# Performance work log

Measured on AMD Instinct MI355X. Metric: run time of the kernel, lower is better.

The kernel has to match this reference:

```python
import jax, jax.numpy as jnp
import numpy as np
from jax import lax

EPS = 1e-6
CLAMP = 1e4


def _ln_last(x, w, b):
    # fp32 LayerNorm over last dim
    mu = jnp.mean(x, axis=-1, keepdims=True)
    var = jnp.mean(jnp.square(x - mu), axis=-1, keepdims=True)
    return (x - mu) * lax.rsqrt(var + EPS) * w + b


def _nan_clean(x):
    return jnp.nan_to_num(x, nan=0.0, posinf=CLAMP, neginf=-CLAMP)


def setup_inputs() -> dict:
    key = jax.random.key(0)
    B, C, H, W = 4, 256, 64, 64
    hid = 2 * C  # expand=2
    k = 3        # d_conv
    ks = jax.random.split(key, 12)
    s = 0.02
    return {
        "x": jax.random.normal(ks[0], (B, C, H, W), jnp.float32),
        "ln2d_w": jnp.ones((C,), jnp.float32),
        "ln2d_b": jnp.zeros((C,), jnp.float32),
        "inproj_w": jax.random.normal(ks[1], (C, C), jnp.float32) * s,
        "inproj_b": jnp.zeros((C,), jnp.float32),
        "dw2d_w": jax.random.normal(ks[2], (C, 3, 3), jnp.float32) * s,
        "dw2d_b": jnp.zeros((C,), jnp.float32),
        "ssm_ln_w": jnp.ones((C,), jnp.float32),
        "ssm_ln_b": jnp.zeros((C,), jnp.float32),
        "ssm_in_w": jax.random.normal(ks[3], (2 * hid, C), jnp.float32) * s,
        "ssm_in_b": jnp.zeros((2 * hid,), jnp.float32),
        "ssm_dw_w": jax.random.normal(ks[4], (hid, k), jnp.float32) * s,
        "ssm_dw_b": jnp.zeros((hid,), jnp.float32),
        "ssm_out_w": jax.random.normal(ks[5], (C, hid), jnp.float32) * s,
        "ssm_out_b": jnp.zeros((C,), jnp.float32),
        "outproj_w": jax.random.normal(ks[6], (C, C), jnp.float32) * s,
        "outproj_b": jnp.zeros((C,), jnp.float32),
    }


def reference(x, ln2d_w, ln2d_b, inproj_w, inproj_b, dw2d_w, dw2d_b,
              ssm_ln_w, ssm_ln_b, ssm_in_w, ssm_in_b, ssm_dw_w, ssm_dw_b,
              ssm_out_w, ssm_out_b, outproj_w, outproj_b):
    B, C, H, W = x.shape
    L = H * W

    # LN2d over channel dim (per-pixel LN on C)
    y = _ln_last(x.transpose(0, 2, 3, 1), ln2d_w, ln2d_b).transpose(0, 3, 1, 2)

    # 1x1 conv in_proj
    y = jnp.einsum('bchw,oc->bohw', y, inproj_w) + inproj_b[None, :, None, None]

    # depthwise 3x3 conv, SAME padding
    y = lax.conv_general_dilated(
        y, dw2d_w[:, None, :, :], (1, 1), ((1, 1), (1, 1)),
        dimension_numbers=('NCHW', 'OIHW', 'NCHW'),
        feature_group_count=C) + dw2d_b[None, :, None, None]

    # cross-scan: 4 routes (B,L,C)
    s0 = y.reshape(B, C, L).transpose(0, 2, 1)                      # row-major
    s1 = s0[:, ::-1]                                                # reversed
    s2 = y.transpose(0, 1, 3, 2).reshape(B, C, L).transpose(0, 2, 1)  # col-major
    s3 = s2[:, ::-1]
    s = jnp.concatenate([s0, s1, s2, s3], axis=0)  # (4B, L, C), shared SSM weights

    # MambaOrLite fallback: LN -> GLU -> depthwise conv1d -> out proj + residual
    r = _ln_last(s, ssm_ln_w, ssm_ln_b)
    r = r @ ssm_in_w.T + ssm_in_b                   # (4B, L, 2*hid)
    a, g = jnp.split(r, 2, axis=-1)
    r = a * jax.nn.sigmoid(g)                       # (4B, L, hid)
    r = r.transpose(0, 2, 1)                        # (4B, hid, L)
    hid = r.shape[1]
    k = ssm_dw_w.shape[-1]
    pad = ((k - 1) // 2, k // 2)
    r = lax.conv_general_dilated(
        r, ssm_dw_w[:, None, :], (1,), (pad,),
        dimension_numbers=('NCH', 'OIH', 'NCH'),
        feature_group_count=hid) + ssm_dw_b[None, :, None]
    r = r.transpose(0, 2, 1) @ ssm_out_w.T + ssm_out_b  # (4B, L, C)
    ys = _nan_clean(r) + s

    # cross-merge: average the 4 routes back to (B,C,H,W)
    y0, y1, y2, y3 = jnp.split(ys, 4, axis=0)
    m0 = y0.transpose(0, 2, 1).reshape(B, C, H, W)
    m1 = y1[:, ::-1].transpose(0, 2, 1).reshape(B, C, H, W)
    m2 = y2.transpose(0, 2, 1).reshape(B, C, W, H).transpose(0, 1, 3, 2)
    m3 = y3[:, ::-1].transpose(0, 2, 1).reshape(B, C, W, H).transpose(0, 1, 3, 2)
    m = (m0 + m1 + m2 + m3) * 0.25

    out = jnp.einsum('bchw,oc->bohw', m, outproj_w) + outproj_b[None, :, None, None]
    out = _nan_clean(out)
    return out + x
```

## Files before the change

### kernel.cpp

```cpp
#include <hip/hip_runtime.h>

typedef float f32x4 __attribute__((ext_vector_type(4)));
typedef __bf16 bf16x8 __attribute__((ext_vector_type(8)));
typedef unsigned short u16;
typedef unsigned int u32;

__device__ __forceinline__ float bf2f(u32 b) {
  u32 x = (b & 0xffffu) << 16;
  return __builtin_bit_cast(float, x);
}
__device__ __forceinline__ u16 f2bf(float f) {
  u32 x = __builtin_bit_cast(u32, f);
  x += 0x7fffu + ((x >> 16) & 1u);
  return (u16)(x >> 16);
}
__device__ __forceinline__ void gload16(const void* g, void* l) {
  __builtin_amdgcn_global_load_lds((__attribute__((address_space(1))) void*)g,
                                   (__attribute__((address_space(3))) void*)l,
                                   16, 0, 0);
}

__global__ __launch_bounds__(256, 2)
void k_ln2d_prep(const float* __restrict__ x, const float* __restrict__ lw,
                 const float* __restrict__ lb, u16* __restrict__ A,
                 const float* __restrict__ inproj_w, const float* __restrict__ ssm_in_w,
                 const float* __restrict__ ssm_out_w, const float* __restrict__ outproj_w,
                 const float* __restrict__ dw2d_w, const float* __restrict__ ssm_dw_w,
                 const float* __restrict__ ssm_dw_b, const float* __restrict__ ssm_out_b,
                 u16* __restrict__ w1b, u16* __restrict__ w2b, u16* __restrict__ w3b,
                 u16* __restrict__ w4b, float* __restrict__ cvec, float* __restrict__ wT9,
                 float* __restrict__ w02, float* __restrict__ w14) {
  __shared__ float T[256 * 65];
  __shared__ float ps1[4][64], ps2[4][64];
  __shared__ float mu[64], rsd[64];
  int bid = blockIdx.x, tid = threadIdx.x;
  if (bid >= 256) {
    int pb = bid - 256;
    if (pb < 512) {
      const float* s; u16* d; int base;
      if (pb < 256)      { s = ssm_in_w;  d = w2b; base = pb; }
      else if (pb < 384) { s = ssm_out_w; d = w3b; base = pb - 256; }
      else if (pb < 448) { s = inproj_w;  d = w1b; base = pb - 384; }
      else               { s = outproj_w; d = w4b; base = pb - 448; }
      int i = base * 1024 + tid * 4;
      float4 v = *(const float4*)&s[i];
      u32 a = (u32)f2bf(v.x) | ((u32)f2bf(v.y) << 16);
      u32 b = (u32)f2bf(v.z) | ((u32)f2bf(v.w) << 16);
      *(uint2*)&d[i] = make_uint2(a, b);
    } else if (pb == 512) {
      float s = ssm_out_b[tid];
      const float* wr = ssm_out_w + (size_t)tid * 512;
      #pragma unroll 8
      for (int k = 0; k < 512; ++k) s += ssm_dw_b[k] * wr[k];
      cvec[tid] = s;
    } else {
      #pragma unroll
      for (int j = 0; j < 9; ++j) wT9[j * 256 + tid] = dw2d_w[tid * 9 + j];
      #pragma unroll
      for (int q = 0; q < 2; ++q) {
        int c = tid + q * 256;
        w02[c] = ssm_dw_w[c * 3 + 0] + ssm_dw_w[c * 3 + 2];
        w14[c] = 4.f * ssm_dw_w[c * 3 + 1];
      }
    }
    return;
  }
  int wv = tid >> 6, lane = tid & 63;
  int cq = lane >> 4, p4 = (lane & 15) * 4;
  int n0 = bid * 64, bb = n0 >> 12, hw0 = n0 & 4095;
  const float* xb = x + ((size_t)bb << 20);
  float s0 = 0, s1 = 0, s2 = 0, s3 = 0;
  float q0 = 0, q1 = 0, q2 = 0, q3 = 0;
  #pragma unroll 4
  for (int i = 0; i < 16; ++i) {
    int c = wv * 64 + i * 4 + cq;
    float4 v = *(const float4*)&xb[((size_t)c << 12) + hw0 + p4];
    T[c * 65 + p4 + 0] = v.x; T[c * 65 + p4 + 1] = v.y;
    T[c * 65 + p4 + 2] = v.z; T[c * 65 + p4 + 3] = v.w;
    s0 += v.x; s1 += v.y; s2 += v.z; s3 += v.w;
    q0 += v.x * v.x; q1 += v.y * v.y; q2 += v.z * v.z; q3 += v.w * v.w;
  }
  #pragma unroll
  for (int off = 16; off < 64; off <<= 1) {
    s0 += __shfl_xor(s0, off); s1 += __shfl_xor(s1, off);
    s2 += __shfl_xor(s2, off); s3 += __shfl_xor(s3, off);
    q0 += __shfl_xor(q0, off); q1 += __shfl_xor(q1, off);
    q2 += __shfl_xor(q2, off); q3 += __shfl_xor(q3, off);
  }
  if (cq == 0) {
    ps1[wv][p4 + 0] = s0; ps1[wv][p4 + 1] = s1; ps1[wv][p4 + 2] = s2; ps1[wv][p4 + 3] = s3;
    ps2[wv][p4 + 0] = q0; ps2[wv][p4 + 1] = q1; ps2[wv][p4 + 2] = q2; ps2[wv][p4 + 3] = q3;
  }
  __syncthreads();
  if (tid < 64) {
    float S1 = ps1[0][tid] + ps1[1][tid] + ps1[2][tid] + ps1[3][tid];
    float S2 = ps2[0][tid] + ps2[1][tid] + ps2[2][tid] + ps2[3][tid];
    float m = S1 * (1.f / 256.f);
    float var = S2 * (1.f / 256.f) - m * m;
    mu[tid] = m;
    rsd[tid] = rsqrtf(var + 1e-6f);
  }
  __syncthreads();
  int c4b = (tid & 15) * 4, p2b = tid >> 4;
  #pragma unroll
  for (int cc = 0; cc < 4; ++cc) {
    int c4 = cc * 64 + c4b;
    float4 w4 = *(const float4*)&lw[c4];
    float4 g4 = *(const float4*)&lb[c4];
    #pragma unroll
    for (int i2 = 0; i2 < 4; ++i2) {
      int p2 = p2b + 16 * i2;
      float m = mu[p2], rs = rsd[p2];
      float o0 = (T[(c4 + 0) * 65 + p2] - m) * rs * w4.x + g4.x;
      float o1 = (T[(c4 + 1) * 65 + p2] - m) * rs * w4.y + g4.y;
      float o2 = (T[(c4 + 2) * 65 + p2] - m) * rs * w4.z + g4.z;
      float o3 = (T[(c4 + 3) * 65 + p2] - m) * rs * w4.w + g4.w;
      u32 a = (u32)f2bf(o0) | ((u32)f2bf(o1) << 16);
      u32 b = (u32)f2bf(o2) | ((u32)f2bf(o3) << 16);
      *(uint2*)&A[(size_t)(n0 + p2) * 256 + c4] = make_uint2(a, b);
    }
  }
}

__global__ __launch_bounds__(256)
void k_dw3x3_ln(const u16* __restrict__ Y1, const float* __restrict__ wT,
                const float* __restrict__ dwb, const float* __restrict__ lnw,
                const float* __restrict__ lnb, u16* __restrict__ Yc,
                u16* __restrict__ A) {
  int tid = threadIdx.x;
  int n = blockIdx.x * 4 + (tid >> 6);
  int lane = tid & 63;
  int c0 = lane * 4;
  int b = n >> 12, hw = n & 4095, h = hw >> 6, w = hw & 63;
  float4 b4 = *(const float4*)&dwb[c0];
  float a0 = b4.x, a1 = b4.y, a2 = b4.z, a3 = b4.w;
  #pragma unroll
  for (int ky = 0; ky < 3; ++ky) {
    int hh = h + ky - 1;
    if (hh < 0 || hh > 63) continue;
    #pragma unroll
    for (int kx = 0; kx < 3; ++kx) {
      int ww = w + kx - 1;
      if (ww < 0 || ww > 63) continue;
      size_t nn = ((size_t)b << 12) + (hh << 6) + ww;
      uint2 u = *(const uint2*)&Y1[nn * 256 + c0];
      float4 w4 = *(const float4*)&wT[(ky * 3 + kx) * 256 + c0];
      a0 += bf2f(u.x) * w4.x;
      a1 += bf2f(u.x >> 16) * w4.y;
      a2 += bf2f(u.y) * w4.z;
      a3 += bf2f(u.y >> 16) * w4.w;
    }
  }
  u32 p0 = (u32)f2bf(a0) | ((u32)f2bf(a1) << 16);
  u32 p1 = (u32)f2bf(a2) | ((u32)f2bf(a3) << 16);
  *(uint2*)&Yc[(size_t)n * 256 + c0] = make_uint2(p0, p1);
  float s1 = a0 + a1 + a2 + a3;
  float s2 = a0 * a0 + a1 * a1 + a2 * a2 + a3 * a3;
  #pragma unroll
  for (int off = 1; off < 64; off <<= 1) {
    s1 += __shfl_xor(s1, off);
    s2 += __shfl_xor(s2, off);
  }
  float m = s1 * (1.f / 256.f);
  float var = s2 * (1.f / 256.f) - m * m;
  float rs = rsqrtf(var + 1e-6f);
  float4 w4 = *(const float4*)&lnw[c0];
  float4 g4 = *(const float4*)&lnb[c0];
  float o0 = (a0 - m) * rs * w4.x + g4.x;
  float o1 = (a1 - m) * rs * w4.y + g4.y;
  float o2 = (a2 - m) * rs * w4.z + g4.z;
  float o3 = (a3 - m) * rs * w4.w + g4.w;
  u32 qa = (u32)f2bf(o0) | ((u32)f2bf(o1) << 16);
  u32 qb = (u32)f2bf(o2) | ((u32)f2bf(o3) << 16);
  *(uint2*)&A[(size_t)n * 256 + c0] = make_uint2(qa, qb);
}

template <int EPI>
__global__ __launch_bounds__(256, 4)
void k_gemm2(const u16* __restrict__ R, const u16* __restrict__ Cm,
             const float* __restrict__ bias, int K, int nCt, int ldo,
             u16* __restrict__ outb, float* __restrict__ outf,
             const float* __restrict__ resf) {
  __shared__ u16 tR[2][64 * 32];
  __shared__ u16 tC[2][128 * 32];
  int tid = threadIdx.x, lane = tid & 63, wv = tid >> 6;
  int rt = blockIdx.x / nCt, ct = blockIdx.x % nCt;
  int r0 = rt * 64, c0 = ct * 128;
  int fr = lane & 15, kc = lane >> 4;
  int sr = lane >> 2, sc = (lane & 3) * 8;
  f32x4 acc[4][2] = {};
  int nK = K >> 5;
  const u16* gR  = R  + (size_t)(r0 + wv * 16 + sr) * K + sc;
  const u16* gC0 = Cm + (size_t)(c0 + wv * 32 + sr) * K + sc;
  const u16* gC1 = Cm + (size_t)(c0 + wv * 32 + 16 + sr) * K + sc;
  auto STAGE = [&](int buf, int kt) {
    int k0 = kt * 32;
    gload16(gR + k0,  &tR[buf][wv * 16 * 32]);
    gload16(gC0 + k0, &tC[buf][(wv * 32) * 32]);
    gload16(gC1 + k0, &tC[buf][(wv * 32 + 16) * 32]);
  };
  auto COMPUTE = [&](int buf) {
    bf16x8 af[4], wf[2];
    #pragma unroll
    for (int m = 0; m < 4; ++m)
      af[m] = *(const bf16x8*)&tR[buf][(m * 16 + fr) * 32 + kc * 8];
    #pragma unroll
    for (int n = 0; n < 2; ++n)
      wf[n] = *(const bf16x8*)&tC[buf][(wv * 32 + n * 16 + fr) * 32 + kc * 8];
    #pragma unroll
    for (int m = 0; m < 4; ++m)
      #pragma unroll
      for (int n = 0; n < 2; ++n)
        acc[m][n] = __builtin_amdgcn_mfma_f32_16x16x32_bf16(af[m], wf[n], acc[m][n], 0, 0, 0);
  };
  STAGE(0, 0);
  __syncthreads();
  int cur = 0;
  for (int kt = 0; kt < nK - 1; ++kt) {
    STAGE(cur ^ 1, kt + 1);
    __builtin_amdgcn_sched_barrier(0);
    COMPUTE(cur);
    __syncthreads();
    cur ^= 1;
  }
  COMPUTE(cur);
  #pragma unroll
  for (int m = 0; m < 4; ++m) {
    #pragma unroll
    for (int n = 0; n < 2; ++n) {
      #pragma unroll
      for (int r = 0; r < 4; ++r) {
        float v = acc[m][n][r];
        if (EPI == 0) {
          int gn = r0 + m * 16 + kc * 4 + r;
          int go = c0 + wv * 32 + n * 16 + fr;
          outb[(size_t)gn * ldo + go] = f2bf(v + bias[go]);
        } else {
          int go = r0 + m * 16 + kc * 4 + r;
          int gn = c0 + wv * 32 + n * 16 + fr;
          int b = gn >> 12, hw = gn & 4095;
          size_t idx = (((size_t)(b * 256 + go)) << 12) + hw;
          outf[idx] = v + bias[go] + resf[idx];
        }
      }
    }
  }
}

__global__ __launch_bounds__(256, 3)
void k_gate2(const u16* __restrict__ A, const u16* __restrict__ W,
             const float* __restrict__ bias, u16* __restrict__ G) {
  __shared__ u16 tR[2][64 * 32];
  __shared__ u16 tCa[2][128 * 32];
  __shared__ u16 tCg[2][128 * 32];
  int tid = threadIdx.x, lane = tid & 63, wv = tid >> 6;
  int rt = blockIdx.x >> 2, ot = blockIdx.x & 3;
  int r0 = rt * 64, o0 = ot * 128;
  int fr = lane & 15, kc = lane >> 4;
  int sr = lane >> 2, sc = (lane & 3) * 8;
  const int K = 256;
  f32x4 acca[4][2] = {}, accg[4][2] = {};
  const u16* gR  = A + (size_t)(r0 + wv * 16 + sr) * K + sc;
  const u16* gA0 = W + (size_t)(o0 + wv * 32 + sr) * K + sc;
  const u16* gA1 = W + (size_t)(o0 + wv * 32 + 16 + sr) * K + sc;
  const u16* gG0 = W + (size_t)(512 + o0 + wv * 32 + sr) * K + sc;
  const u16* gG1 = W + (size_t)(512 + o0 + wv * 32 + 16 + sr) * K + sc;
  auto STAGE = [&](int buf, int kt) {
    int k0 = kt * 32;
    gload16(gR + k0,  &tR[buf][wv * 16 * 32]);
    gload16(gA0 + k0, &tCa[buf][(wv * 32) * 32]);
    gload16(gA1 + k0, &tCa[buf][(wv * 32 + 16) * 32]);
    gload16(gG0 + k0, &tCg[buf][(wv * 32) * 32]);
    gload16(gG1 + k0, &tCg[buf][(wv * 32 + 16) * 32]);
  };
  auto COMPUTE = [&](int buf) {
    bf16x8 af[4], wa[2], wg[2];
    #pragma unroll
    for (int m = 0; m < 4; ++m)
      af[m] = *(const bf16x8*)&tR[buf][(m * 16 + fr) * 32 + kc * 8];
    #pragma unroll
    for (int n = 0; n < 2; ++n) {
      wa[n] = *(const bf16x8*)&tCa[buf][(wv * 32 + n * 16 + fr) * 32 + kc * 8];
      wg[n] = *(const bf16x8*)&tCg[buf][(wv * 32 + n * 16 + fr) * 32 + kc * 8];
    }
    #pragma unroll
    for (int m = 0; m < 4; ++m)
      #pragma unroll
      for (int n = 0; n < 2; ++n) {
        acca[m][n] = __builtin_amdgcn_mfma_f32_16x16x32_bf16(af[m], wa[n], acca[m][n], 0, 0, 0);
        accg[m][n] = __builtin_amdgcn_mfma_f32_16x16x32_bf16(af[m], wg[n], accg[m][n], 0, 0, 0);
      }
  };
  STAGE(0, 0);
  __syncthreads();
  int cur = 0;
  for (int kt = 0; kt < 7; ++kt) {
    STAGE(cur ^ 1, kt + 1);
    __builtin_amdgcn_sched_barrier(0);
    COMPUTE(cur);
    __syncthreads();
    cur ^= 1;
  }
  COMPUTE(cur);
  #pragma unroll
  for (int m = 0; m < 4; ++m) {
    #pragma unroll
    for (int n = 0; n < 2; ++n) {
      #pragma unroll
      for (int r = 0; r < 4; ++r) {
        int gn = r0 + m * 16 + kc * 4 + r;
        int go = o0 + wv * 32 + n * 16 + fr;
        float a = acca[m][n][r] + bias[go];
        float g = accg[m][n][r] + bias[512 + go];
        G[(size_t)gn * 512 + go] = f2bf(a / (1.f + expf(-g)));
      }
    }
  }
}

__global__ __launch_bounds__(256, 2)
void k_gemm_scan(const u16* __restrict__ G, const u16* __restrict__ W3,
                 const float* __restrict__ w02, const float* __restrict__ w14,
                 const float* __restrict__ cvec, const u16* __restrict__ Yc,
                 u16* __restrict__ M) {
  __shared__ u16 tR[2][32 * 32];
  __shared__ u16 tC[2][256 * 32];
  int tid = threadIdx.x, lane = tid & 63, wv = tid >> 6;
  int r0 = blockIdx.x * 32;
  int fr = lane & 15, kc = lane >> 4;
  int zrow = tid >> 3;
  int zg = (tid & 7) * 4;
  int n = r0 + zrow;
  int b = n >> 12, hw = n & 4095, h = hw >> 6, w = hw & 63;
  int m = w * 64 + h;
  int mm1 = m - 1, mp1 = m + 1;
  size_t o_c = (size_t)n * 512 + zg;
  size_t o_p = (size_t)(hw > 0 ? n - 1 : n) * 512 + zg;
  size_t o_n = (size_t)(hw < 4095 ? n + 1 : n) * 512 + zg;
  size_t o_u = (size_t)(m > 0 ? ((b << 12) + ((mm1 & 63) << 6) + (mm1 >> 6)) : n) * 512 + zg;
  size_t o_d = (size_t)(m < 4095 ? ((b << 12) + ((mp1 & 63) << 6) + (mp1 >> 6)) : n) * 512 + zg;
  float mP = hw > 0 ? 1.f : 0.f, mN = hw < 4095 ? 1.f : 0.f;
  float mU = m > 0 ? 1.f : 0.f, mD = m < 4095 ? 1.f : 0.f;
  f32x4 acc[2][4] = {};
  auto STAGE_C = [&](int buf, int kt) {
    int k0 = kt * 32;
    #pragma unroll
    for (int i = 0; i < 4; ++i) {
      int s0 = wv * 256 + i * 64;
      int s = s0 + lane;
      int row = s >> 2, off = (s & 3) * 8;
      gload16(W3 + (size_t)row * 512 + k0 + off, &tC[buf][s0 * 8]);
    }
  };
  uint2 lc, lp, ln_, lu, ld;
  float4 va, vb;
  auto ZLOAD = [&](int kt) {
    int c = kt * 32 + zg;
    lc = *(const uint2*)&G[o_c + (kt * 32)];
    lp = *(const uint2*)&G[o_p + (kt * 32)];
    ln_ = *(const uint2*)&G[o_n + (kt * 32)];
    lu = *(const uint2*)&G[o_u + (kt * 32)];
    ld = *(const uint2*)&G[o_d + (kt * 32)];
    va = *(const float4*)&w02[c];
    vb = *(const float4*)&w14[c];
  };
  auto ZSTORE = [&](int buf) {
    float s_0 = mP * bf2f(lp.x) + mN * bf2f(ln_.x) + mU * bf2f(lu.x) + mD * bf2f(ld.x);
    float s_1 = mP * bf2f(lp.x >> 16) + mN * bf2f(ln_.x >> 16) + mU * bf2f(lu.x >> 16) + mD * bf2f(ld.x >> 16);
    float s_2 = mP * bf2f(lp.y) + mN * bf2f(ln_.y) + mU * bf2f(lu.y) + mD * bf2f(ld.y);
    float s_3 = mP * bf2f(lp.y >> 16) + mN * bf2f(ln_.y >> 16) + mU * bf2f(lu.y >> 16) + mD * bf2f(ld.y >> 16);
    float z0 = va.x * s_0 + vb.x * bf2f(lc.x);
    float z1 = va.y * s_1 + vb.y * bf2f(lc.x >> 16);
    float z2 = va.z * s_2 + vb.z * bf2f(lc.y);
    float z3 = va.w * s_3 + vb.w * bf2f(lc.y >> 16);
    u32 p0 = (u32)f2bf(z0) | ((u32)f2bf(z1) << 16);
    u32 p1 = (u32)f2bf(z2) | ((u32)f2bf(z3) << 16);
    *(uint2*)&tR[buf][zrow * 32 + zg] = make_uint2(p0, p1);
  };
  auto COMPUTE = [&](int buf) {
    bf16x8 af[2], wf[4];
    #pragma unroll
    for (int mi = 0; mi < 2; ++mi)
      af[mi] = *(const bf16x8*)&tR[buf][(mi * 16 + fr) * 32 + kc * 8];
    #pragma unroll
    for (int ni = 0; ni < 4; ++ni)
      wf[ni] = *(const bf16x8*)&tC[buf][(wv * 64 + ni * 16 + fr) * 32 + kc * 8];
    #pragma unroll
    for (int mi = 0; mi < 2; ++mi)
      #pragma unroll
      for (int ni = 0; ni < 4; ++ni)
        acc[mi][ni] = __builtin_amdgcn_mfma_f32_16x16x32_bf16(af[mi], wf[ni], acc[mi][ni], 0, 0, 0);
  };
  STAGE_C(0, 0);
  ZLOAD(0);
  ZSTORE(0);
  __syncthreads();
  int cur = 0;
  for (int kt = 0; kt < 15; ++kt) {
    ZLOAD(kt + 1);
    STAGE_C(cur ^ 1, kt + 1);
    COMPUTE(cur);
    ZSTORE(cur ^ 1);
    __syncthreads();
    cur ^= 1;
  }
  COMPUTE(cur);
  #pragma unroll
  for (int mi = 0; mi < 2; ++mi) {
    #pragma unroll
    for (int ni = 0; ni < 4; ++ni) {
      #pragma unroll
      for (int r = 0; r < 4; ++r) {
        int gn = r0 + mi * 16 + kc * 4 + r;
        int go = wv * 64 + ni * 16 + fr;
        size_t idx = (size_t)gn * 256 + go;
        M[idx] = f2bf(0.25f * acc[mi][ni][r] + cvec[go] + bf2f(Yc[idx]));
      }
    }
  }
}

extern "C" void kernel_launch(void* const* d_in, const int* in_sizes, int n_in,
                              void* d_out, int out_size, void* d_ws, size_t ws_size,
                              hipStream_t stream) {
  const float* x         = (const float*)d_in[0];
  const float* ln2d_w    = (const float*)d_in[1];
  const float* ln2d_b    = (const float*)d_in[2];
  const float* inproj_w  = (const float*)d_in[3];
  const float* inproj_b  = (const float*)d_in[4];
  const float* dw2d_w    = (const float*)d_in[5];
  const float* dw2d_b    = (const float*)d_in[6];
  const float* ssm_ln_w  = (const float*)d_in[7];
  const float* ssm_ln_b  = (const float*)d_in[8];
  const float* ssm_in_w  = (const float*)d_in[9];
  const float* ssm_in_b  = (const float*)d_in[10];
  const float* ssm_dw_w  = (const float*)d_in[11];
  const float* ssm_dw_b  = (const float*)d_in[12];
  const float* ssm_out_w = (const float*)d_in[13];
  const float* ssm_out_b = (const float*)d_in[14];
  const float* outproj_w = (const float*)d_in[15];
  const float* outproj_b = (const float*)d_in[16];
  float* out = (float*)d_out;

  char* ws = (char*)d_ws;
  size_t off = 0;
  auto take = [&](size_t bytes) -> char* {
    char* p = ws + off;
    off = (off + bytes + 255) & ~(size_t)255;
    return p;
  };
  u16* w1b    = (u16*)take(65536 * 2);
  u16* w2b    = (u16*)take(262144 * 2);
  u16* w3b    = (u16*)take(131072 * 2);
  u16* w4b    = (u16*)take(65536 * 2);
  float* cvec = (float*)take(256 * 4);
  float* wT9  = (float*)take(9 * 256 * 4);
  float* w02  = (float*)take(512 * 4);
  float* w14  = (float*)take(512 * 4);
  u16* Abuf   = (u16*)take((size_t)16384 * 256 * 2);
  u16* Y1     = (u16*)take((size_t)16384 * 256 * 2);
  u16* Yc     = (u16*)take((size_t)16384 * 256 * 2);
  u16* G      = (u16*)take((size_t)16384 * 512 * 2);
  (void)ws_size; (void)in_sizes; (void)n_in; (void)out_size;

  k_ln2d_prep<<<770, 256, 0, stream>>>(x, ln2d_w, ln2d_b, Abuf,
                                       inproj_w, ssm_in_w, ssm_out_w, outproj_w,
                                       dw2d_w, ssm_dw_w, ssm_dw_b, ssm_out_b,
                                       w1b, w2b, w3b, w4b, cvec, wT9, w02, w14);
  k_gemm2<0><<<512, 256, 0, stream>>>(Abuf, w1b, inproj_b, 256, 2, 256,
                                      Y1, nullptr, nullptr);
  k_dw3x3_ln<<<4096, 256, 0, stream>>>(Y1, wT9, dw2d_b, ssm_ln_w, ssm_ln_b, Yc, Abuf);
  k_gate2<<<1024, 256, 0, stream>>>(Abuf, w2b, ssm_in_b, G);
  k_gemm_scan<<<512, 256, 0, stream>>>(G, w3b, w02, w14, cvec, Yc, Abuf);
  k_gemm2<2><<<512, 256, 0, stream>>>(w4b, Abuf, outproj_b, 256, 128, 0,
                                      nullptr, out, x);
}
```

Measured before the change: 105.7 us.

## Fuse output projection GEMM into scan kernel and add XCD block swizzle

Fuses the final outproj GEMM, bias and residual add into the scan/ssm_out kernel. The merged 32x256 tile is kept in swizzled LDS and multiplied by the bf16 outproj weights read straight from global memory, so the intermediate M buffer no longer makes a round trip through HBM and one launch is removed. Also specializes the input GEMM to a fixed K and adds an XCD-aware block index swizzle to the depthwise and scan kernels for L2 locality. The cost is extra LDS per block (16KB) and W4 fragments loaded from global without staging, which may lower occupancy and add memory latency.

```diff
diff --git a/kernel.cpp b/kernel.cpp
--- a/kernel.cpp
+++ b/kernel.cpp
@@ -18,6 +18,10 @@
   __builtin_amdgcn_global_load_lds((__attribute__((address_space(1))) void*)g,
                                    (__attribute__((address_space(3))) void*)l,
                                    16, 0, 0);
+}
+__device__ __forceinline__ int xcd_swz(int bid, int nwg) {
+  int per = nwg >> 3;
+  return (bid & 7) * per + (bid >> 3);
 }
 
 __global__ __launch_bounds__(256, 2)
@@ -122,13 +126,74 @@
   }
 }
 
+__global__ __launch_bounds__(256, 4)
+void k_gemm_in(const u16* __restrict__ R, const u16* __restrict__ Cm,
+               const float* __restrict__ bias, u16* __restrict__ outb) {
+  __shared__ u16 tR[2][64 * 32];
+  __shared__ u16 tC[2][128 * 32];
+  int tid = threadIdx.x, lane = tid & 63, wv = tid >> 6;
+  const int K = 256;
+  int rt = blockIdx.x >> 1, ct = blockIdx.x & 1;
+  int r0 = rt * 64, c0 = ct * 128;
+  int fr = lane & 15, kc = lane >> 4;
+  int sr = lane >> 2, sc = (lane & 3) * 8;
+  f32x4 acc[4][2] = {};
+  const u16* gR  = R  + (size_t)(r0 + wv * 16 + sr) * K + sc;
+  const u16* gC0 = Cm + (size_t)(c0 + wv * 32 + sr) * K + sc;
+  const u16* gC1 = Cm + (size_t)(c0 + wv * 32 + 16 + sr) * K + sc;
+  auto STAGE = [&](int buf, int kt) {
+    int k0 = kt * 32;
+    gload16(gR + k0,  &tR[buf][wv * 16 * 32]);
+    gload16(gC0 + k0, &tC[buf][(wv * 32) * 32]);
+    gload16(gC1 + k0, &tC[buf][(wv * 32 + 16) * 32]);
+  };
+  auto COMPUTE = [&](int buf) {
+    bf16x8 af[4], wf[2];
+    #pragma unroll
+    for (int m = 0; m < 4; ++m)
+      af[m] = *(const bf16x8*)&tR[buf][(m * 16 + fr) * 32 + kc * 8];
+    #pragma unroll
+    for (int n = 0; n < 2; ++n)
+      wf[n] = *(const bf16x8*)&tC[buf][(wv * 32 + n * 16 + fr) * 32 + kc * 8];
+    #pragma unroll
+    for (int m = 0; m < 4; ++m)
+      #pragma unroll
+      for (int n = 0; n < 2; ++n)
+        acc[m][n] = __builtin_amdgcn_mfma_f32_16x16x32_bf16(af[m], wf[n], acc[m][n], 0, 0, 0);
+  };
+  STAGE(0, 0);
+  __syncthreads();
+  int cur = 0;
+  for (int kt = 0; kt < 7; ++kt) {
+    STAGE(cur ^ 1, kt + 1);
+    __builtin_amdgcn_sched_barrier(0);
+    COMPUTE(cur);
+    __syncthreads();
+    cur ^= 1;
+  }
+  COMPUTE(cur);
+  #pragma unroll
+  for (int m = 0; m < 4; ++m) {
+    #pragma unroll
+    for (int n = 0; n < 2; ++n) {
+      #pragma unroll
+      for (int r = 0; r < 4; ++r) {
+        int gn = r0 + m * 16 + kc * 4 + r;
+        int go = c0 + wv * 32 + n * 16 + fr;
+        outb[(size_t)gn * 256 + go] = f2bf(acc[m][n][r] + bias[go]);
+      }
+    }
+  }
+}
+
 __global__ __launch_bounds__(256)
 void k_dw3x3_ln(const u16* __restrict__ Y1, const float* __restrict__ wT,
                 const float* __restrict__ dwb, const float* __restrict__ lnw,
                 const float* __restrict__ lnb, u16* __restrict__ Yc,
                 u16* __restrict__ A) {
   int tid = threadIdx.x;
-  int n = blockIdx.x * 4 + (tid >> 6);
+  int wg = xcd_swz(blockIdx.x, 4096);
+  int n = wg * 4 + (tid >> 6);
   int lane = tid & 63;
   int c0 = lane * 4;
   int b = n >> 12, hw = n & 4095, h = hw >> 6, w = hw & 63;
@@ -173,78 +238,6 @@
   u32 qa = (u32)f2bf(o0) | ((u32)f2bf(o1) << 16);
   u32 qb = (u32)f2bf(o2) | ((u32)f2bf(o3) << 16);
   *(uint2*)&A[(size_t)n * 256 + c0] = make_uint2(qa, qb);
-}
-
-template <int EPI>
-__global__ __launch_bounds__(256, 4)
-void k_gemm2(const u16* __restrict__ R, const u16* __restrict__ Cm,
-             const float* __restrict__ bias, int K, int nCt, int ldo,
-             u16* __restrict__ outb, float* __restrict__ outf,
-             const float* __restrict__ resf) {
-  __shared__ u16 tR[2][64 * 32];
-  __shared__ u16 tC[2][128 * 32];
-  int tid = threadIdx.x, lane = tid & 63, wv = tid >> 6;
-  int rt = blockIdx.x / nCt, ct = blockIdx.x % nCt;
-  int r0 = rt * 64, c0 = ct * 128;
-  int fr = lane & 15, kc = lane >> 4;
-  int sr = lane >> 2, sc = (lane & 3) * 8;
-  f32x4 acc[4][2] = {};
-  int nK = K >> 5;
-  const u16* gR  = R  + (size_t)(r0 + wv * 16 + sr) * K + sc;
-  const u16* gC0 = Cm + (size_t)(c0 + wv * 32 + sr) * K + sc;
-  const u16* gC1 = Cm + (size_t)(c0 + wv * 32 + 16 + sr) * K + sc;
-  auto STAGE = [&](int buf, int kt) {
-    int k0 = kt * 32;
-    gload16(gR + k0,  &tR[buf][wv * 16 * 32]);
-    gload16(gC0 + k0, &tC[buf][(wv * 32) * 32]);
-    gload16(gC1 + k0, &tC[buf][(wv * 32 + 16) * 32]);
-  };
-  auto COMPUTE = [&](int buf) {
-    bf16x8 af[4], wf[2];
-    #pragma unroll
-    for (int m = 0; m < 4; ++m)
-      af[m] = *(const bf16x8*)&tR[buf][(m * 16 + fr) * 32 + kc * 8];
-    #pragma unroll
-    for (int n = 0; n < 2; ++n)
-      wf[n] = *(const bf16x8*)&tC[buf][(wv * 32 + n * 16 + fr) * 32 + kc * 8];
-    #pragma unroll
-    for (int m = 0; m < 4; ++m)
-      #pragma unroll
-      for (int n = 0; n < 2; ++n)
-        acc[m][n] = __builtin_amdgcn_mfma_f32_16x16x32_bf16(af[m], wf[n], acc[m][n], 0, 0, 0);
-  };
-  STAGE(0, 0);
-  __syncthreads();
-  int cur = 0;
-  for (int kt = 0; kt < nK - 1; ++kt) {
-    STAGE(cur ^ 1, kt + 1);
-    __builtin_amdgcn_sched_barrier(0);
-    COMPUTE(cur);
-    __syncthreads();
-    cur ^= 1;
-  }
-  COMPUTE(cur);
-  #pragma unroll
-  for (int m = 0; m < 4; ++m) {
-    #pragma unroll
-    for (int n = 0; n < 2; ++n) {
-      #pragma unroll
-      for (int r = 0; r < 4; ++r) {
-        float v = acc[m][n][r];
-        if (EPI == 0) {
-          int gn = r0 + m * 16 + kc * 4 + r;
-          int go = c0 + wv * 32 + n * 16 + fr;
-          outb[(size_t)gn * ldo + go] = f2bf(v + bias[go]);
-        } else {
-          int go = r0 + m * 16 + kc * 4 + r;
-          int gn = c0 + wv * 32 + n * 16 + fr;
-          int b = gn >> 12, hw = gn & 4095;
-          size_t idx = (((size_t)(b * 256 + go)) << 12) + hw;
-          outf[idx] = v + bias[go] + resf[idx];
-        }
-      }
-    }
-  }
 }
 
 __global__ __launch_bounds__(256, 3)
@@ -319,14 +312,17 @@
 }
 
 __global__ __launch_bounds__(256, 2)
-void k_gemm_scan(const u16* __restrict__ G, const u16* __restrict__ W3,
-                 const float* __restrict__ w02, const float* __restrict__ w14,
-                 const float* __restrict__ cvec, const u16* __restrict__ Yc,
-                 u16* __restrict__ M) {
+void k_scan_out(const u16* __restrict__ G, const u16* __restrict__ W3,
+                const float* __restrict__ w02, const float* __restrict__ w14,
+                const float* __restrict__ cvec, const u16* __restrict__ Yc,
+                const u16* __restrict__ W4, const float* __restrict__ outb,
+                const float* __restrict__ xres, float* __restrict__ out) {
   __shared__ u16 tR[2][32 * 32];
   __shared__ u16 tC[2][256 * 32];
+  __shared__ u16 sM[32 * 256];
   int tid = threadIdx.x, lane = tid & 63, wv = tid >> 6;
-  int r0 = blockIdx.x * 32;
+  int wg = xcd_swz(blockIdx.x, 512);
+  int r0 = wg * 32;
   int fr = lane & 15, kc = lane >> 4;
   int zrow = tid >> 3;
   int zg = (tid & 7) * 4;
@@ -356,11 +352,11 @@
   float4 va, vb;
   auto ZLOAD = [&](int kt) {
     int c = kt * 32 + zg;
-    lc = *(const uint2*)&G[o_c + (kt * 32)];
-    lp = *(const uint2*)&G[o_p + (kt * 32)];
+    lc  = *(const uint2*)&G[o_c + (kt * 32)];
+    lp  = *(const uint2*)&G[o_p + (kt * 32)];
     ln_ = *(const uint2*)&G[o_n + (kt * 32)];
-    lu = *(const uint2*)&G[o_u + (kt * 32)];
-    ld = *(const uint2*)&G[o_d + (kt * 32)];
+    lu  = *(const uint2*)&G[o_u + (kt * 32)];
+    ld  = *(const uint2*)&G[o_d + (kt * 32)];
     va = *(const float4*)&w02[c];
     vb = *(const float4*)&w14[c];
   };
@@ -411,10 +407,47 @@
     for (int ni = 0; ni < 4; ++ni) {
       #pragma unroll
       for (int r = 0; r < 4; ++r) {
-        int gn = r0 + mi * 16 + kc * 4 + r;
+        int row = mi * 16 + kc * 4 + r;
         int go = wv * 64 + ni * 16 + fr;
-        size_t idx = (size_t)gn * 256 + go;
-        M[idx] = f2bf(0.25f * acc[mi][ni][r] + cvec[go] + bf2f(Yc[idx]));
+        float mval = 0.25f * acc[mi][ni][r] + cvec[go] +
+                     bf2f(Yc[(size_t)(r0 + row) * 256 + go]);
+        u32 ba = ((u32)(row * 512 + go * 2)) ^ ((u32)(row & 7) << 4);
+        *(u16*)((char*)sM + ba) = f2bf(mval);
+      }
+    }
+  }
+  __syncthreads();
+  f32x4 acc2[4][2] = {};
+  #pragma unroll 2
+  for (int kt = 0; kt < 8; ++kt) {
+    bf16x8 af2[4], bfv[2];
+    #pragma unroll
+    for (int mi = 0; mi < 4; ++mi)
+      af2[mi] = *(const bf16x8*)&W4[(size_t)(wv * 64 + mi * 16 + fr) * 256 + kt * 32 + kc * 8];
+    #pragma unroll
+    for (int ni = 0; ni < 2; ++ni) {
+      int pos = ni * 16 + fr;
+      u32 ba = ((u32)(pos * 512 + (kt * 32 + kc * 8) * 2)) ^ ((u32)(pos & 7) << 4);
+      bfv[ni] = *(const bf16x8*)((const char*)sM + ba);
+    }
+    #pragma unroll
+    for (int mi = 0; mi < 4; ++mi)
+      #pragma unroll
+      for (int ni = 0; ni < 2; ++ni)
+        acc2[mi][ni] = __builtin_amdgcn_mfma_f32_16x16x32_bf16(af2[mi], bfv[ni], acc2[mi][ni], 0, 0, 0);
+  }
+  int bb = r0 >> 12, hwb = r0 & 4095;
+  #pragma unroll
+  for (int mi = 0; mi < 4; ++mi) {
+    #pragma unroll
+    for (int ni = 0; ni < 2; ++ni) {
+      #pragma unroll
+      for (int r = 0; r < 4; ++r) {
+        int o = wv * 64 + mi * 16 + kc * 4 + r;
+        int pos = ni * 16 + fr;
+        size_t idx = (((size_t)(bb * 256 + o)) << 12) + hwb + pos;
+        float res = __builtin_nontemporal_load(&xres[idx]);
+        __builtin_nontemporal_store(acc2[mi][ni][r] + outb[o] + res, &out[idx]);
       }
     }
   }
@@ -467,11 +500,9 @@
                                        inproj_w, ssm_in_w, ssm_out_w, outproj_w,
                                        dw2d_w, ssm_dw_w, ssm_dw_b, ssm_out_b,
                                        w1b, w2b, w3b, w4b, cvec, wT9, w02, w14);
-  k_gemm2<0><<<512, 256, 0, stream>>>(Abuf, w1b, inproj_b, 256, 2, 256,
-                                      Y1, nullptr, nullptr);
+  k_gemm_in<<<512, 256, 0, stream>>>(Abuf, w1b, inproj_b, Y1);
   k_dw3x3_ln<<<4096, 256, 0, stream>>>(Y1, wT9, dw2d_b, ssm_ln_w, ssm_ln_b, Yc, Abuf);
   k_gate2<<<1024, 256, 0, stream>>>(Abuf, w2b, ssm_in_b, G);
-  k_gemm_scan<<<512, 256, 0, stream>>>(G, w3b, w02, w14, cvec, Yc, Abuf);
-  k_gemm2<2><<<512, 256, 0, stream>>>(w4b, Abuf, outproj_b, 256, 128, 0,
-                                      nullptr, out, x);
-}
+  k_scan_out<<<512, 256, 0, stream>>>(G, w3b, w02, w14, cvec, Yc,
+                                      w4b, outproj_b, x, out);
+}
```

Result: slower. 109.6 us (+3.8%).
